# Performance work log

Measured on AMD Instinct MI355X. Metric: run time of the kernel, lower is better.

Reference implementation:

```python
import jax, jax.numpy as jnp
import numpy as np

B, LP, LR = 16, 128, 1024
D = 128
DG = 640  # 5 * 128 concat
K = 7     # number of FC trans heads
EDGE_P = 0.05


def _gcn_block(x, adj, mask, W1, b1, W2, b2):
    # x: [B,L,DG], adj: [B,L,L] (nonzero => edge weight 1, like dense_to_sparse + GCNConv)
    A = (adj != 0).astype(x.dtype)
    L = A.shape[-1]
    eye = jnp.eye(L, dtype=x.dtype)
    Ah = jnp.maximum(A, eye)                     # add_remaining_self_loops
    deg = Ah.sum(axis=1)                         # col degree [B,L] (gcn_norm uses target index)
    dinv = jax.lax.rsqrt(deg)                    # deg >= 1 thanks to self loops
    N = Ah * dinv[:, :, None] * dinv[:, None, :] # normalized adjacency per edge (r,c)
    agg = lambda h: jnp.einsum('brc,brd->bcd', N, h)  # aggregate sources r into target c
    h1 = jax.nn.relu(agg(x @ W1) + b1)
    h2 = agg(h1 @ W2) + b2
    return jax.nn.relu(x + h2) * mask[..., None]


def _fc_trans(feature, Wt, bt):
    # feature: [B,L,DG]; Wt: [K,D,DG]; bt: [K,D]
    h = jnp.einsum('bld,kod->kblo', feature, Wt) + bt[:, None, None, :]
    h = jax.nn.relu(h)                 # FCNet [640->128], ReLU (dropout off in eval)
    return jnp.swapaxes(h, 2, 3)       # [K,B,D,L] (transpose(1,2))


def _forward(x_pep, x_ss_pep, x_2_pep, x_dense_pep, x_pretrain_pep,
             x_pro, x_ss_pro, x_2_pro, x_dense_pro, x_pretrain_pro,
             x_edge_pep, x_edge_pro, x_seqmask_pep, x_seqmask_pro,
             E_seq, E_ss, E_two, W_dpep, b_dpep, W_dpro, b_dpro,
             W_ppep, b_ppep, W_ppro, b_ppro,
             Wg_pep1, bg_pep1, Wg_pep2, bg_pep2,
             Wg_pro1, bg_pro1, Wg_pro2, bg_pro2,
             Wt_pep, bt_pep, Wt_pro, bt_pro):
    enc_pep = jnp.concatenate([
        E_seq[x_pep], E_ss[x_ss_pep], E_two[x_2_pep],
        x_dense_pep @ W_dpep + b_dpep,
        x_pretrain_pep @ W_ppep + b_ppep], axis=-1) * x_seqmask_pep[..., None]
    enc_pro = jnp.concatenate([
        E_seq[x_pro], E_ss[x_ss_pro], E_two[x_2_pro],
        x_dense_pro @ W_dpro + b_dpro,
        x_pretrain_pro @ W_ppro + b_ppro], axis=-1) * x_seqmask_pro[..., None]

    f_pep = _gcn_block(enc_pep, x_edge_pep, x_seqmask_pep, Wg_pep1, bg_pep1, Wg_pep2, bg_pep2)
    f_pro = _gcn_block(enc_pro, x_edge_pro, x_seqmask_pro, Wg_pro1, bg_pro1, Wg_pro2, bg_pro2)

    pep_vecs = _fc_trans(f_pep, Wt_pep, bt_pep)[..., None]        # [K,B,D,LP,1] (unsqueeze 3)
    pro_vecs = _fc_trans(f_pro, Wt_pro, bt_pro)[:, :, :, None, :]  # [K,B,D,1,LR] (unsqueeze 2)
    return pep_vecs, pro_vecs


def setup_inputs() -> dict:
    key = jax.random.key(0)
    ks = jax.random.split(key, 40)
    f32 = jnp.float32
    s = 0.05
    inp = {
        'x_pep': jax.random.randint(ks[0], (B, LP), 0, 25),
        'x_ss_pep': jax.random.randint(ks[1], (B, LP), 0, 73),
        'x_2_pep': jax.random.randint(ks[2], (B, LP), 0, 8),
        'x_dense_pep': jax.random.normal(ks[3], (B, LP, 3), f32),
        'x_pretrain_pep': jax.random.normal(ks[4], (B, LP, 1024), f32),
        'x_pro': jax.random.randint(ks[5], (B, LR), 0, 25),
        'x_ss_pro': jax.random.randint(ks[6], (B, LR), 0, 73),
        'x_2_pro': jax.random.randint(ks[7], (B, LR), 0, 8),
        'x_dense_pro': jax.random.normal(ks[8], (B, LR, 23), f32),
        'x_pretrain_pro': jax.random.normal(ks[9], (B, LR, 1024), f32),
        'x_edge_pep': (jax.random.uniform(ks[10], (B, LP, LP)) < EDGE_P).astype(f32),
        'x_edge_pro': (jax.random.uniform(ks[11], (B, LR, LR)) < EDGE_P).astype(f32),
        'x_seqmask_pep': jnp.ones((B, LP), f32),
        'x_seqmask_pro': jnp.ones((B, LR), f32),
        'E_seq': jax.random.normal(ks[12], (25, D), f32) * s,
        'E_ss': jax.random.normal(ks[13], (73, D), f32) * s,
        'E_two': jax.random.normal(ks[14], (8, D), f32) * s,
        'W_dpep': jax.random.normal(ks[15], (3, D), f32) * s,
        'b_dpep': jnp.zeros((D,), f32),
        'W_dpro': jax.random.normal(ks[16], (23, D), f32) * s,
        'b_dpro': jnp.zeros((D,), f32),
        'W_ppep': jax.random.normal(ks[17], (1024, D), f32) * s,
        'b_ppep': jnp.zeros((D,), f32),
        'W_ppro': jax.random.normal(ks[18], (1024, D), f32) * s,
        'b_ppro': jnp.zeros((D,), f32),
        'Wg_pep1': jax.random.normal(ks[19], (DG, DG), f32) * s,
        'bg_pep1': jnp.zeros((DG,), f32),
        'Wg_pep2': jax.random.normal(ks[20], (DG, DG), f32) * s,
        'bg_pep2': jnp.zeros((DG,), f32),
        'Wg_pro1': jax.random.normal(ks[21], (DG, DG), f32) * s,
        'bg_pro1': jnp.zeros((DG,), f32),
        'Wg_pro2': jax.random.normal(ks[22], (DG, DG), f32) * s,
        'bg_pro2': jnp.zeros((DG,), f32),
        'Wt_pep': jax.random.normal(ks[23], (K, D, DG), f32) * s,
        'bt_pep': jnp.zeros((K, D), f32),
        'Wt_pro': jax.random.normal(ks[24], (K, D, DG), f32) * s,
        'bt_pro': jnp.zeros((K, D), f32),
    }
    return inp


def reference(x_pep, x_ss_pep, x_2_pep, x_dense_pep, x_pretrain_pep,
              x_pro, x_ss_pro, x_2_pro, x_dense_pro, x_pretrain_pro,
              x_edge_pep, x_edge_pro, x_seqmask_pep, x_seqmask_pro,
              E_seq, E_ss, E_two, W_dpep, b_dpep, W_dpro, b_dpro,
              W_ppep, b_ppep, W_ppro, b_ppro,
              Wg_pep1, bg_pep1, Wg_pep2, bg_pep2,
              Wg_pro1, bg_pro1, Wg_pro2, bg_pro2,
              Wt_pep, bt_pep, Wt_pro, bt_pro):
    return _forward(x_pep, x_ss_pep, x_2_pep, x_dense_pep, x_pretrain_pep,
                    x_pro, x_ss_pro, x_2_pro, x_dense_pro, x_pretrain_pro,
                    x_edge_pep, x_edge_pro, x_seqmask_pep, x_seqmask_pro,
                    E_seq, E_ss, E_two, W_dpep, b_dpep, W_dpro, b_dpro,
                    W_ppep, b_ppep, W_ppro, b_ppro,
                    Wg_pep1, bg_pep1, Wg_pep2, bg_pep2,
                    Wg_pro1, bg_pro1, Wg_pro2, bg_pro2,
                    Wt_pep, bt_pep, Wt_pro, bt_pro)
```

## Files before the change

kernel.cpp:

```cpp
#include <hip/hip_runtime.h>
#include <hip/hip_bf16.h>

#define BSZ 16
#define LP 128
#define LR 1024
#define DD 128
#define DG 640
#define KH 7
#define SPLITK 4

typedef __bf16 bf16x8 __attribute__((ext_vector_type(8)));
typedef __bf16 bf16x4v __attribute__((ext_vector_type(4)));
typedef float f32x4 __attribute__((ext_vector_type(4)));
typedef unsigned int uint32;

__device__ __forceinline__ void gl16(const void* g, void* l) {
  __builtin_amdgcn_global_load_lds(
      (const __attribute__((address_space(1))) unsigned int*)g,
      (__attribute__((address_space(3))) unsigned int*)l, 16, 0, 0);
}

__device__ __forceinline__ void mfma_core_lds(
    const ushort* __restrict__ Ab, int lda,
    const ushort* __restrict__ Bb, int ldb,
    int m0, int n0, int kStart, int kEnd, f32x4 (&acc)[4][4]) {
  __shared__ __align__(16) ushort As[128 * 64];
  __shared__ __align__(16) ushort Bs[128 * 64];
  int t = threadIdx.x;
  int wave = t >> 6, lane = t & 63;
  int quad = lane >> 4, l16 = lane & 15;
  int wm = (wave >> 1) * 64, wn = (wave & 1) * 64;

  int row0 = (wave * 256 + lane) >> 3;
  int s0 = lane & 7;
  const ushort* aBase = Ab + (size_t)(m0 + row0) * lda + s0 * 8;
  const ushort* bBase = Bb + (size_t)(n0 + row0) * ldb + s0 * 8;

  for (int k0 = kStart; k0 < kEnd; k0 += 64) {
    #pragma unroll
    for (int i = 0; i < 4; ++i) {
      gl16(aBase + (size_t)i * 8 * lda + k0, &As[wave * 2048 + i * 512]);
      gl16(bBase + (size_t)i * 8 * ldb + k0, &Bs[wave * 2048 + i * 512]);
    }
    __syncthreads();
    #pragma unroll
    for (int kc = 0; kc < 2; ++kc) {
      bf16x8 af[4], bfr[4];
      #pragma unroll
      for (int fi = 0; fi < 4; ++fi)
        af[fi] = *(const bf16x8*)&As[(wm + fi * 16 + l16) * 64 + kc * 32 + quad * 8];
      #pragma unroll
      for (int fj = 0; fj < 4; ++fj)
        bfr[fj] = *(const bf16x8*)&Bs[(wn + fj * 16 + l16) * 64 + kc * 32 + quad * 8];
      #pragma unroll
      for (int fi = 0; fi < 4; ++fi)
        #pragma unroll
        for (int fj = 0; fj < 4; ++fj)
          acc[fi][fj] = __builtin_amdgcn_mfma_f32_16x16x32_bf16(
              af[fi], bfr[fj], acc[fi][fj], 0, 0, 0);
    }
    __syncthreads();
  }
}

__device__ __forceinline__ void mfma_core_f32(
    const float* __restrict__ Af, int lda,
    const ushort* __restrict__ Bb, int ldb,
    int m0, int n0, int kStart, int kEnd, f32x4 (&acc)[4][4]) {
  __shared__ __align__(16) ushort As[128 * 72];
  __shared__ __align__(16) ushort Bs[128 * 72];
  int t = threadIdx.x;
  int wave = t >> 6, lane = t & 63;
  int quad = lane >> 4, l16 = lane & 15;
  int wm = (wave >> 1) * 64, wn = (wave & 1) * 64;
  int r1 = t >> 2, o1 = (t & 3) * 16;

  int4 b00, b01, b10, b11;
  float4 af32[8];

  auto load_k = [&](int k0) {
    b00 = *(const int4*)(Bb + (size_t)(n0 + r1) * ldb + k0 + o1);
    b01 = *(const int4*)(Bb + (size_t)(n0 + r1) * ldb + k0 + o1 + 8);
    b10 = *(const int4*)(Bb + (size_t)(n0 + r1 + 64) * ldb + k0 + o1);
    b11 = *(const int4*)(Bb + (size_t)(n0 + r1 + 64) * ldb + k0 + o1 + 8);
    #pragma unroll
    for (int s = 0; s < 8; ++s) {
      int idx = t + s * 256;
      int row = idx >> 4, c4 = (idx & 15) * 4;
      af32[s] = *(const float4*)(Af + (size_t)(m0 + row) * lda + k0 + c4);
    }
  };

  load_k(kStart);
  for (int k0 = kStart; k0 < kEnd; k0 += 64) {
    __syncthreads();
    #pragma unroll
    for (int s = 0; s < 8; ++s) {
      int idx = t + s * 256;
      int row = idx >> 4, c4 = (idx & 15) * 4;
      ushort4 u; __bf16 h;
      h = (__bf16)af32[s].x; u.x = *(ushort*)&h;
      h = (__bf16)af32[s].y; u.y = *(ushort*)&h;
      h = (__bf16)af32[s].z; u.z = *(ushort*)&h;
      h = (__bf16)af32[s].w; u.w = *(ushort*)&h;
      *(ushort4*)&As[row * 72 + c4] = u;
    }
    *(int4*)&Bs[r1 * 72 + o1] = b00;
    *(int4*)&Bs[r1 * 72 + o1 + 8] = b01;
    *(int4*)&Bs[(r1 + 64) * 72 + o1] = b10;
    *(int4*)&Bs[(r1 + 64) * 72 + o1 + 8] = b11;
    __syncthreads();
    if (k0 + 64 < kEnd) load_k(k0 + 64);
    #pragma unroll
    for (int kc = 0; kc < 2; ++kc) {
      bf16x8 af[4], bfr[4];
      #pragma unroll
      for (int fi = 0; fi < 4; ++fi)
        af[fi] = *(const bf16x8*)&As[(wm + fi * 16 + l16) * 72 + kc * 32 + quad * 8];
      #pragma unroll
      for (int fj = 0; fj < 4; ++fj)
        bfr[fj] = *(const bf16x8*)&Bs[(wn + fj * 16 + l16) * 72 + kc * 32 + quad * 8];
      #pragma unroll
      for (int fi = 0; fi < 4; ++fi)
        #pragma unroll
        for (int fj = 0; fj < 4; ++fj)
          acc[fi][fj] = __builtin_amdgcn_mfma_f32_16x16x32_bf16(
              af[fi], bfr[fj], acc[fi][fj], 0, 0, 0);
    }
  }
}

__device__ __forceinline__ void agg_core(
    const uint32* __restrict__ pb, int L,
    const ushort* __restrict__ Bb, int ldb,
    int m0, int n0, f32x4 (&acc)[4][4]) {
  __shared__ __align__(16) ushort Bs[128 * 64];
  __shared__ uint32 Aw[2][128];
  int t = threadIdx.x;
  int wave = t >> 6, lane = t & 63;
  int quad = lane >> 4, l16 = lane & 15;
  int wm = (wave >> 1) * 64, wn = (wave & 1) * 64;
  int half = t >> 7, cc = t & 127;

  int row0 = (wave * 256 + lane) >> 3;
  int s0 = lane & 7;
  const ushort* bBase = Bb + (size_t)(n0 + row0) * ldb + s0 * 8;
  const uint32* pbBase = pb + (size_t)half * L + m0 + cc;

  for (int k0 = 0; k0 < L; k0 += 64) {
    #pragma unroll
    for (int i = 0; i < 4; ++i)
      gl16(bBase + (size_t)i * 8 * ldb + k0, &Bs[wave * 2048 + i * 512]);
    Aw[half][cc] = pbBase[(size_t)(k0 >> 5) * L];
    __syncthreads();
    #pragma unroll
    for (int kc = 0; kc < 2; ++kc) {
      bf16x8 af[4], bfr[4];
      #pragma unroll
      for (int fj = 0; fj < 4; ++fj)
        bfr[fj] = *(const bf16x8*)&Bs[(wn + fj * 16 + l16) * 64 + kc * 32 + quad * 8];
      #pragma unroll
      for (int fi = 0; fi < 4; ++fi) {
        uint32 bits = (Aw[kc][wm + fi * 16 + l16] >> (quad * 8)) & 0xffu;
        int4 p;
        p.x = (int)((((bits >> 0) & 1) ? 0x3F80u : 0u) | (((bits >> 1) & 1) ? 0x3F800000u : 0u));
        p.y = (int)((((bits >> 2) & 1) ? 0x3F80u : 0u) | (((bits >> 3) & 1) ? 0x3F800000u : 0u));
        p.z = (int)((((bits >> 4) & 1) ? 0x3F80u : 0u) | (((bits >> 5) & 1) ? 0x3F800000u : 0u));
        p.w = (int)((((bits >> 6) & 1) ? 0x3F80u : 0u) | (((bits >> 7) & 1) ? 0x3F800000u : 0u));
        af[fi] = *(bf16x8*)&p;
      }
      #pragma unroll
      for (int fi = 0; fi < 4; ++fi)
        #pragma unroll
        for (int fj = 0; fj < 4; ++fj)
          acc[fi][fj] = __builtin_amdgcn_mfma_f32_16x16x32_bf16(
              af[fi], bfr[fj], acc[fi][fj], 0, 0, 0);
    }
    __syncthreads();
  }
}

__device__ __forceinline__ void tr_tile(const float* __restrict__ src,
                                        __bf16* __restrict__ dst,
                                        int R, int C, int cb, int rb, int t) {
  __shared__ float T[32][33];
  int r0 = rb * 32, c0 = cb * 32;
  #pragma unroll
  for (int s = 0; s < 4; ++s) {
    int idx = t + s * 256;
    int r = idx >> 5, c = idx & 31;
    T[r][c] = src[(size_t)(r0 + r) * C + c0 + c];
  }
  __syncthreads();
  #pragma unroll
  for (int s = 0; s < 4; ++s) {
    int idx = t + s * 256;
    int c = idx >> 5, r = idx & 31;
    dst[(size_t)(c0 + c) * R + r0 + r] = (__bf16)T[r][c];
  }
}

__global__ __launch_bounds__(256) void prep_weights(
    const float* __restrict__ Wppep, const float* __restrict__ Wppro,
    const float* __restrict__ Wg1p, const float* __restrict__ Wg2p,
    const float* __restrict__ Wg1r, const float* __restrict__ Wg2r,
    const float* __restrict__ Wtp, const float* __restrict__ Wtr,
    __bf16* __restrict__ WppTp, __bf16* __restrict__ WppTr,
    __bf16* __restrict__ Wg1Tp, __bf16* __restrict__ Wg2Tp,
    __bf16* __restrict__ Wg1Tr, __bf16* __restrict__ Wg2Tr,
    __bf16* __restrict__ WtBp, __bf16* __restrict__ WtBr) {
  int z = blockIdx.z, bx = blockIdx.x, t = threadIdx.x;
  if (z < 2) {
    if (bx >= 128) return;
    tr_tile(z ? Wppro : Wppep, z ? WppTr : WppTp, 1024, 128, bx % 4, bx / 4, t);
  } else if (z < 6) {
    if (bx >= 400) return;
    const float* src = (z == 2) ? Wg1p : (z == 3) ? Wg2p : (z == 4) ? Wg1r : Wg2r;
    __bf16* dst = (z == 2) ? Wg1Tp : (z == 3) ? Wg2Tp : (z == 4) ? Wg1Tr : Wg2Tr;
    tr_tile(src, dst, 640, 640, bx % 20, bx / 20, t);
  } else {
    if (bx >= 560) return;
    const float* src = (z == 6) ? Wtp : Wtr;
    __bf16* dst = (z == 6) ? WtBp : WtBr;
    int i = bx * 256 + t;
    float4 v = ((const float4*)src)[i];
    bf16x4v o;
    o.x = (__bf16)v.x; o.y = (__bf16)v.y; o.z = (__bf16)v.z; o.w = (__bf16)v.w;
    ((bf16x4v*)dst)[i] = o;
  }
}

__global__ __launch_bounds__(256) void zero_f32(float* __restrict__ p, int n) {
  int i = blockIdx.x * 256 + threadIdx.x;
  if (i < n) p[i] = 0.f;
}

__global__ __launch_bounds__(256) void rsqrt_k(const float* __restrict__ deg,
                                               float* __restrict__ dinv, int n) {
  int i = blockIdx.x * 256 + threadIdx.x;
  if (i < n) dinv[i] = rsqrtf(deg[i]);
}

__global__ __launch_bounds__(256) void prep_pack_merged(
    const float* __restrict__ adjP, const float* __restrict__ adjR,
    uint32* __restrict__ packedP, uint32* __restrict__ packedR,
    float* __restrict__ degP, float* __restrict__ degR) {
  int t = threadIdx.x;
  const float* adj; uint32* packed; float* deg;
  int b, rw, c, L;
  if (blockIdx.z < 16) {
    L = LR; b = blockIdx.z; rw = blockIdx.y; c = blockIdx.x * 256 + t;
    adj = adjR; packed = packedR; deg = degR;
  } else {
    L = LP; b = blockIdx.y; rw = blockIdx.x; c = t;
    if (b >= 16 || c >= LP) return;
    adj = adjP; packed = packedP; deg = degP;
  }
  const float* adjB = adj + (size_t)b * L * L;
  uint32 w = 0;
  int rbase = rw * 32;
  #pragma unroll 8
  for (int j = 0; j < 32; ++j) {
    float a = adjB[(size_t)(rbase + j) * L + c];
    if (a != 0.f || (rbase + j) == c) w |= (1u << j);
  }
  packed[((size_t)b * (L >> 5) + rw) * L + c] = w;
  atomicAdd(deg + b * L + c, (float)__popc(w));
}

__global__ __launch_bounds__(256) void pre_gemm(
    const float* __restrict__ XpP, const float* __restrict__ XpR,
    const __bf16* __restrict__ WppTp, const __bf16* __restrict__ WppTr,
    float* __restrict__ partP, float* __restrict__ partR) {
  int bx = blockIdx.x, s = blockIdx.y;
  int pep = bx < (BSZ * LP / 128);
  int m0 = (pep ? bx : bx - BSZ * LP / 128) * 128;
  const float* A = pep ? XpP : XpR;
  const ushort* B = (const ushort*)(pep ? WppTp : WppTr);
  int BL = pep ? BSZ * LP : BSZ * LR;
  float* part = (pep ? partP : partR) + (size_t)s * BL * DD;

  f32x4 acc[4][4];
  #pragma unroll
  for (int i = 0; i < 4; ++i)
    #pragma unroll
    for (int j = 0; j < 4; ++j) acc[i][j] = (f32x4){0.f, 0.f, 0.f, 0.f};
  mfma_core_f32(A, 1024, B, 1024, m0, 0, s * (1024 / SPLITK),
                (s + 1) * (1024 / SPLITK), acc);

  int t = threadIdx.x;
  int wave = t >> 6, lane = t & 63;
  int quad = lane >> 4, l16 = lane & 15;
  int wm = (wave >> 1) * 64, wn = (wave & 1) * 64;
  #pragma unroll
  for (int fi = 0; fi < 4; ++fi)
    #pragma unroll
    for (int r = 0; r < 4; ++r) {
      int m = m0 + wm + fi * 16 + quad * 4 + r;
      #pragma unroll
      for (int fj = 0; fj < 4; ++fj) {
        int n = wn + fj * 16 + l16;
        part[(size_t)m * DD + n] = acc[fi][fj][r];
      }
    }
}

__global__ __launch_bounds__(128) void encoder_merged(
    const int* __restrict__ xsP, const int* __restrict__ xssP,
    const int* __restrict__ x2P, const float* __restrict__ xdP,
    const float* __restrict__ WdP, const float* __restrict__ bdP,
    const float* __restrict__ maskP, const float* __restrict__ partP,
    const float* __restrict__ bppP, __bf16* __restrict__ encP,
    const int* __restrict__ xsR, const int* __restrict__ xssR,
    const int* __restrict__ x2R, const float* __restrict__ xdR,
    const float* __restrict__ WdR, const float* __restrict__ bdR,
    const float* __restrict__ maskR, const float* __restrict__ partR,
    const float* __restrict__ bppR, __bf16* __restrict__ encR,
    const float* __restrict__ Eseq, const float* __restrict__ Ess,
    const float* __restrict__ Etwo) {
  int gw = blockIdx.x;
  int t = threadIdx.x;
  int pep = gw < BSZ * LP;
  int row = pep ? gw : gw - BSZ * LP;
  int BL = pep ? BSZ * LP : BSZ * LR;
  int Kd = pep ? 3 : 23;
  const int* xs = pep ? xsP : xsR;
  const int* xss = pep ? xssP : xssR;
  const int* x2 = pep ? x2P : x2R;
  const float* xd = pep ? xdP : xdR;
  const float* Wd = pep ? WdP : WdR;
  const float* bd = pep ? bdP : bdR;
  const float* mask = pep ? maskP : maskR;
  const float* part = pep ? partP : partR;
  const float* bpp = pep ? bppP : bppR;
  __bf16* enc = pep ? encP : encR;

  float m = mask[row];
  int i0 = xs[row], i1 = xss[row], i2 = x2[row];
  __bf16* e = enc + (size_t)row * DG;
  e[t]        = (__bf16)(Eseq[i0 * DD + t] * m);
  e[DD + t]   = (__bf16)(Ess[i1 * DD + t] * m);
  e[2*DD + t] = (__bf16)(Etwo[i2 * DD + t] * m);
  float acc = bd[t];
  const float* xr = xd + (size_t)row * Kd;
  for (int i = 0; i < Kd; ++i) acc = fmaf(xr[i], Wd[i * DD + t], acc);
  e[3*DD + t] = (__bf16)(acc * m);
  float p = bpp[t];
  #pragma unroll
  for (int s = 0; s < SPLITK; ++s)
    p += part[(size_t)s * BL * DD + (size_t)row * DD + t];
  e[4*DD + t] = (__bf16)(p * m);
}

__global__ __launch_bounds__(256) void linT_merged(
    const __bf16* __restrict__ WgTp, const __bf16* __restrict__ srcP,
    const float* __restrict__ dinvP, __bf16* __restrict__ dstP,
    const __bf16* __restrict__ WgTr, const __bf16* __restrict__ srcR,
    const float* __restrict__ dinvR, __bf16* __restrict__ dstR) {
  int bx = blockIdx.x;
  int pep = bx < (BSZ * LP / 128);
  int n0 = (pep ? bx : bx - BSZ * LP / 128) * 128;
  int m0 = blockIdx.y * 128;
  int BL = pep ? BSZ * LP : BSZ * LR;
  const ushort* A = (const ushort*)(pep ? WgTp : WgTr);
  const ushort* B = (const ushort*)(pep ? srcP : srcR);
  const float* dinv = pep ? dinvP : dinvR;
  __bf16* dst = pep ? dstP : dstR;

  f32x4 acc[4][4];
  #pragma unroll
  for (int i = 0; i < 4; ++i)
    #pragma unroll
    for (int j = 0; j < 4; ++j) acc[i][j] = (f32x4){0.f, 0.f, 0.f, 0.f};
  mfma_core_lds(A, DG, B, DG, m0, n0, 0, DG, acc);

  int t = threadIdx.x;
  int wave = t >> 6, lane = t & 63;
  int quad = lane >> 4, l16 = lane & 15;
  int wm = (wave >> 1) * 64, wn = (wave & 1) * 64;
  #pragma unroll
  for (int fi = 0; fi < 4; ++fi)
    #pragma unroll
    for (int r = 0; r < 4; ++r) {
      int m = m0 + wm + fi * 16 + quad * 4 + r;
      #pragma unroll
      for (int fj = 0; fj < 4; ++fj) {
        int n = n0 + wn + fj * 16 + l16;
        dst[(size_t)m * BL + n] = (__bf16)(acc[fi][fj][r] * dinv[n]);
      }
    }
}

__global__ __launch_bounds__(256) void agg_merged(
    const uint32* __restrict__ packedP, const __bf16* __restrict__ XtP,
    const float* __restrict__ dinvP, const float* __restrict__ biasP,
    const __bf16* __restrict__ encEP, const float* __restrict__ maskP,
    __bf16* __restrict__ YP,
    const uint32* __restrict__ packedR, const __bf16* __restrict__ XtR,
    const float* __restrict__ dinvR, const float* __restrict__ biasR,
    const __bf16* __restrict__ encER, const float* __restrict__ maskR,
    __bf16* __restrict__ YR) {
  int bx = blockIdx.x;
  int b = bx / 5;
  int n0 = (bx % 5) * 128;
  int pep = (blockIdx.y == 0);
  int L = pep ? LP : LR;
  int BL = BSZ * L;
  int m0 = pep ? 0 : (blockIdx.y - 1) * 128;
  const uint32* pb = (pep ? packedP : packedR) + (size_t)b * (L >> 5) * L;
  const ushort* Bb = (const ushort*)(pep ? XtP : XtR) + (size_t)b * L;
  const float* dinv = pep ? dinvP : dinvR;
  const float* bias = pep ? biasP : biasR;
  const __bf16* encE = pep ? encEP : encER;
  const float* mask = pep ? maskP : maskR;
  __bf16* Y = pep ? YP : YR;

  f32x4 acc[4][4];
  #pragma unroll
  for (int i = 0; i < 4; ++i)
    #pragma unroll
    for (int j = 0; j < 4; ++j) acc[i][j] = (f32x4){0.f, 0.f, 0.f, 0.f};
  agg_core(pb, L, Bb, BL, m0, n0, acc);

  int t = threadIdx.x;
  int wave = t >> 6, lane = t & 63;
  int quad = lane >> 4, l16 = lane & 15;
  int wm = (wave >> 1) * 64, wn = (wave & 1) * 64;
  int gRow = b * L;
  #pragma unroll
  for (int fi = 0; fi < 4; ++fi)
    #pragma unroll
    for (int r = 0; r < 4; ++r) {
      int m = m0 + wm + fi * 16 + quad * 4 + r;
      int gi = gRow + m;
      float di = dinv[gi];
      float rm = mask ? mask[gi] : 1.f;
      #pragma unroll
      for (int fj = 0; fj < 4; ++fj) {
        int n = n0 + wn + fj * 16 + l16;
        float v = acc[fi][fj][r] * di + bias[n];
        if (encE) v += (float)encE[(size_t)gi * DG + n];
        v = fmaxf(v, 0.f);
        v *= rm;
        Y[(size_t)gi * DG + n] = (__bf16)v;
      }
    }
}

__global__ __launch_bounds__(256) void fct_merged(
    const __bf16* __restrict__ WtBp, const float* __restrict__ btp,
    const __bf16* __restrict__ Yp, float* __restrict__ outP,
    const __bf16* __restrict__ WtBr, const float* __restrict__ btr,
    const __bf16* __restrict__ Yr, float* __restrict__ outR) {
  int kh = blockIdx.y;
  int pro = (blockIdx.z < 16);
  const ushort* A;
  const ushort* B;
  const float* bt;
  int n0;
  if (pro) {
    A = (const ushort*)(WtBr + (size_t)kh * DD * DG);
    B = (const ushort*)(Yr + (size_t)blockIdx.z * LR * DG);
    bt = btr;
    n0 = blockIdx.x * 128;
  } else {
    A = (const ushort*)(WtBp + (size_t)kh * DD * DG);
    B = (const ushort*)Yp;
    bt = btp;
    n0 = ((blockIdx.z - 16) * 8 + blockIdx.x) * 128;
  }

  f32x4 acc[4][4];
  #pragma unroll
  for (int i = 0; i < 4; ++i)
    #pragma unroll
    for (int j = 0; j < 4; ++j) acc[i][j] = (f32x4){0.f, 0.f, 0.f, 0.f};
  mfma_core_lds(A, DG, B, DG, 0, n0, 0, DG, acc);

  int t = threadIdx.x;
  int wave = t >> 6, lane = t & 63;
  int quad = lane >> 4, l16 = lane & 15;
  int wm = (wave >> 1) * 64, wn = (wave & 1) * 64;
  #pragma unroll
  for (int fi = 0; fi < 4; ++fi)
    #pragma unroll
    for (int r = 0; r < 4; ++r) {
      int m = wm + fi * 16 + quad * 4 + r;
      float bb = bt[kh * DD + m];
      #pragma unroll
      for (int fj = 0; fj < 4; ++fj) {
        int n = n0 + wn + fj * 16 + l16;
        float v = fmaxf(acc[fi][fj][r] + bb, 0.f);
        if (pro) {
          outR[((size_t)(kh * BSZ + blockIdx.z) * DD + m) * LR + n] = v;
        } else {
          int b = n >> 7, l = n & 127;
          outP[((size_t)(kh * BSZ + b) * DD + m) * LP + l] = v;
        }
      }
    }
}

extern "C" void kernel_launch(void* const* d_in, const int* in_sizes, int n_in,
                              void* d_out, int out_size, void* d_ws, size_t ws_size,
                              hipStream_t stream) {
  const int*   x_pep          = (const int*)d_in[0];
  const int*   x_ss_pep       = (const int*)d_in[1];
  const int*   x_2_pep        = (const int*)d_in[2];
  const float* x_dense_pep    = (const float*)d_in[3];
  const float* x_pretrain_pep = (const float*)d_in[4];
  const int*   x_pro          = (const int*)d_in[5];
  const int*   x_ss_pro       = (const int*)d_in[6];
  const int*   x_2_pro        = (const int*)d_in[7];
  const float* x_dense_pro    = (const float*)d_in[8];
  const float* x_pretrain_pro = (const float*)d_in[9];
  const float* x_edge_pep     = (const float*)d_in[10];
  const float* x_edge_pro     = (const float*)d_in[11];
  const float* mask_pep       = (const float*)d_in[12];
  const float* mask_pro       = (const float*)d_in[13];
  const float* E_seq          = (const float*)d_in[14];
  const float* E_ss           = (const float*)d_in[15];
  const float* E_two          = (const float*)d_in[16];
  const float* W_dpep         = (const float*)d_in[17];
  const float* b_dpep         = (const float*)d_in[18];
  const float* W_dpro         = (const float*)d_in[19];
  const float* b_dpro         = (const float*)d_in[20];
  const float* W_ppep         = (const float*)d_in[21];
  const float* b_ppep         = (const float*)d_in[22];
  const float* W_ppro         = (const float*)d_in[23];
  const float* b_ppro         = (const float*)d_in[24];
  const float* Wg_pep1        = (const float*)d_in[25];
  const float* bg_pep1        = (const float*)d_in[26];
  const float* Wg_pep2        = (const float*)d_in[27];
  const float* bg_pep2        = (const float*)d_in[28];
  const float* Wg_pro1        = (const float*)d_in[29];
  const float* bg_pro1        = (const float*)d_in[30];
  const float* Wg_pro2        = (const float*)d_in[31];
  const float* bg_pro2        = (const float*)d_in[32];
  const float* Wt_pep         = (const float*)d_in[33];
  const float* bt_pep         = (const float*)d_in[34];
  const float* Wt_pro         = (const float*)d_in[35];
  const float* bt_pro         = (const float*)d_in[36];

  float* out = (float*)d_out;
  const int BLp = BSZ * LP;
  const int BLr = BSZ * LR;
  const size_t out_pro_off = (size_t)KH * BSZ * DD * LP;

  char* w = (char*)d_ws;
  __bf16* encBp  = (__bf16*)w; w += (size_t)BLp * DG * 2;
  __bf16* encBr  = (__bf16*)w; w += (size_t)BLr * DG * 2;
  __bf16* bufATp = (__bf16*)w; w += (size_t)DG * BLp * 2;
  __bf16* bufATr = (__bf16*)w; w += (size_t)DG * BLr * 2;
  __bf16* bufYp  = (__bf16*)w; w += (size_t)BLp * DG * 2;
  __bf16* bufYr  = (__bf16*)w; w += (size_t)BLr * DG * 2;
  __bf16* WppTp  = (__bf16*)w; w += (size_t)DD * 1024 * 2;
  __bf16* WppTr  = (__bf16*)w; w += (size_t)DD * 1024 * 2;
  __bf16* Wg1Tp  = (__bf16*)w; w += (size_t)DG * DG * 2;
  __bf16* Wg2Tp  = (__bf16*)w; w += (size_t)DG * DG * 2;
  __bf16* Wg1Tr  = (__bf16*)w; w += (size_t)DG * DG * 2;
  __bf16* Wg2Tr  = (__bf16*)w; w += (size_t)DG * DG * 2;
  __bf16* WtBp   = (__bf16*)w; w += (size_t)KH * DD * DG * 2;
  __bf16* WtBr   = (__bf16*)w; w += (size_t)KH * DD * DG * 2;
  uint32* packedP = (uint32*)w; w += (size_t)BSZ * (LP / 32) * LP * 4;
  uint32* packedR = (uint32*)w; w += (size_t)BSZ * (LR / 32) * LR * 4;
  float* degP  = (float*)w; w += (size_t)BLp * 4;
  float* degR  = (float*)w; w += (size_t)BLr * 4;
  float* dinvP = (float*)w; w += (size_t)BLp * 4;
  float* dinvR = (float*)w; w += (size_t)BLr * 4;
  float* partP = (float*)w; w += (size_t)SPLITK * BLp * DD * 4;
  float* partR = (float*)w; w += (size_t)SPLITK * BLr * DD * 4;

  prep_weights<<<dim3(560, 1, 8), 256, 0, stream>>>(
      W_ppep, W_ppro, Wg_pep1, Wg_pep2, Wg_pro1, Wg_pro2, Wt_pep, Wt_pro,
      WppTp, WppTr, Wg1Tp, Wg2Tp, Wg1Tr, Wg2Tr, WtBp, WtBr);
  zero_f32<<<(BLp + BLr) / 256, 256, 0, stream>>>(degP, BLp + BLr);
  prep_pack_merged<<<dim3(4, 32, 17), 256, 0, stream>>>(
      x_edge_pep, x_edge_pro, packedP, packedR, degP, degR);
  rsqrt_k<<<(BLp + BLr) / 256, 256, 0, stream>>>(degP, dinvP, BLp + BLr);
  pre_gemm<<<dim3((BLp + BLr) / 128, SPLITK), 256, 0, stream>>>(
      x_pretrain_pep, x_pretrain_pro, WppTp, WppTr, partP, partR);
  encoder_merged<<<BLp + BLr, 128, 0, stream>>>(
      x_pep, x_ss_pep, x_2_pep, x_dense_pep, W_dpep, b_dpep, mask_pep, partP,
      b_ppep, encBp,
      x_pro, x_ss_pro, x_2_pro, x_dense_pro, W_dpro, b_dpro, mask_pro, partR,
      b_ppro, encBr,
      E_seq, E_ss, E_two);
  linT_merged<<<dim3((BLp + BLr) / 128, DG / 128), 256, 0, stream>>>(
      Wg1Tp, encBp, dinvP, bufATp, Wg1Tr, encBr, dinvR, bufATr);
  agg_merged<<<dim3(80, 9), 256, 0, stream>>>(
      packedP, bufATp, dinvP, bg_pep1, nullptr, nullptr, bufYp,
      packedR, bufATr, dinvR, bg_pro1, nullptr, nullptr, bufYr);
  linT_merged<<<dim3((BLp + BLr) / 128, DG / 128), 256, 0, stream>>>(
      Wg2Tp, bufYp, dinvP, bufATp, Wg2Tr, bufYr, dinvR, bufATr);
  agg_merged<<<dim3(80, 9), 256, 0, stream>>>(
      packedP, bufATp, dinvP, bg_pep2, encBp, mask_pep, bufYp,
      packedR, bufATr, dinvR, bg_pro2, encBr, mask_pro, bufYr);
  fct_merged<<<dim3(LR / 128, KH, 18), 256, 0, stream>>>(
      WtBp, bt_pep, bufYp, out,
      WtBr, bt_pro, bufYr, out + out_pro_off);
}
```

Measured before the change: 495.8 us.

## Halve GEMM N-tile to 64 and switch to register-prefetched padded LDS staging

Replaces the 128x128 MFMA tiles in the linear, aggregation and FC-trans kernels with 128x64 tiles, doubling grid sizes so more blocks fill the GPU. It also drops the direct global-to-LDS loads in favour of register prefetch of the next K slice, stored into padded (stride 72) LDS to avoid bank conflicts and overlap loads with MFMA compute. The cost is lower per-block data reuse, so each operand is read from memory more often.

```diff
diff --git a/kernel.cpp b/kernel.cpp
--- a/kernel.cpp
+++ b/kernel.cpp
@@ -14,52 +14,110 @@
 typedef float f32x4 __attribute__((ext_vector_type(4)));
 typedef unsigned int uint32;
 
-__device__ __forceinline__ void gl16(const void* g, void* l) {
-  __builtin_amdgcn_global_load_lds(
-      (const __attribute__((address_space(1))) unsigned int*)g,
-      (__attribute__((address_space(3))) unsigned int*)l, 16, 0, 0);
-}
-
-__device__ __forceinline__ void mfma_core_lds(
+__device__ __forceinline__ void mfma_core_n64(
     const ushort* __restrict__ Ab, int lda,
     const ushort* __restrict__ Bb, int ldb,
-    int m0, int n0, int kStart, int kEnd, f32x4 (&acc)[4][4]) {
-  __shared__ __align__(16) ushort As[128 * 64];
-  __shared__ __align__(16) ushort Bs[128 * 64];
+    int m0, int n0, int kStart, int kEnd, f32x4 (&acc)[2][4]) {
+  __shared__ __align__(16) ushort As[128 * 72];
+  __shared__ __align__(16) ushort Bs[64 * 72];
   int t = threadIdx.x;
   int wave = t >> 6, lane = t & 63;
   int quad = lane >> 4, l16 = lane & 15;
-  int wm = (wave >> 1) * 64, wn = (wave & 1) * 64;
-
-  int row0 = (wave * 256 + lane) >> 3;
-  int s0 = lane & 7;
-  const ushort* aBase = Ab + (size_t)(m0 + row0) * lda + s0 * 8;
-  const ushort* bBase = Bb + (size_t)(n0 + row0) * ldb + s0 * 8;
-
+  int wm = wave * 32;
+  int r1 = t >> 2, o1 = (t & 3) * 16;
+
+  int4 a0, a1, a2, a3, bb0, bb1;
+  auto load_k = [&](int k0) {
+    a0 = *(const int4*)(Ab + (size_t)(m0 + r1) * lda + k0 + o1);
+    a1 = *(const int4*)(Ab + (size_t)(m0 + r1) * lda + k0 + o1 + 8);
+    a2 = *(const int4*)(Ab + (size_t)(m0 + r1 + 64) * lda + k0 + o1);
+    a3 = *(const int4*)(Ab + (size_t)(m0 + r1 + 64) * lda + k0 + o1 + 8);
+    bb0 = *(const int4*)(Bb + (size_t)(n0 + r1) * ldb + k0 + o1);
+    bb1 = *(const int4*)(Bb + (size_t)(n0 + r1) * ldb + k0 + o1 + 8);
+  };
+
+  load_k(kStart);
   for (int k0 = kStart; k0 < kEnd; k0 += 64) {
-    #pragma unroll
-    for (int i = 0; i < 4; ++i) {
-      gl16(aBase + (size_t)i * 8 * lda + k0, &As[wave * 2048 + i * 512]);
-      gl16(bBase + (size_t)i * 8 * ldb + k0, &Bs[wave * 2048 + i * 512]);
-    }
     __syncthreads();
+    *(int4*)&As[r1 * 72 + o1] = a0;
+    *(int4*)&As[r1 * 72 + o1 + 8] = a1;
+    *(int4*)&As[(r1 + 64) * 72 + o1] = a2;
+    *(int4*)&As[(r1 + 64) * 72 + o1 + 8] = a3;
+    *(int4*)&Bs[r1 * 72 + o1] = bb0;
+    *(int4*)&Bs[r1 * 72 + o1 + 8] = bb1;
+    __syncthreads();
+    if (k0 + 64 < kEnd) load_k(k0 + 64);
     #pragma unroll
     for (int kc = 0; kc < 2; ++kc) {
-      bf16x8 af[4], bfr[4];
-      #pragma unroll
-      for (int fi = 0; fi < 4; ++fi)
-        af[fi] = *(const bf16x8*)&As[(wm + fi * 16 + l16) * 64 + kc * 32 + quad * 8];
+      bf16x8 af[2], bfr[4];
+      #pragma unroll
+      for (int fi = 0; fi < 2; ++fi)
+        af[fi] = *(const bf16x8*)&As[(wm + fi * 16 + l16) * 72 + kc * 32 + quad * 8];
       #pragma unroll
       for (int fj = 0; fj < 4; ++fj)
-        bfr[fj] = *(const bf16x8*)&Bs[(wn + fj * 16 + l16) * 64 + kc * 32 + quad * 8];
-      #pragma unroll
-      for (int fi = 0; fi < 4; ++fi)
+        bfr[fj] = *(const bf16x8*)&Bs[(fj * 16 + l16) * 72 + kc * 32 + quad * 8];
+      #pragma unroll
+      for (int fi = 0; fi < 2; ++fi)
         #pragma unroll
         for (int fj = 0; fj < 4; ++fj)
           acc[fi][fj] = __builtin_amdgcn_mfma_f32_16x16x32_bf16(
               af[fi], bfr[fj], acc[fi][fj], 0, 0, 0);
     }
+  }
+}
+
+__device__ __forceinline__ void agg_core_n64(
+    const uint32* __restrict__ pb, int L,
+    const ushort* __restrict__ Bb, int ldb,
+    int m0, int n0, f32x4 (&acc)[2][4]) {
+  __shared__ __align__(16) ushort Bs[64 * 72];
+  __shared__ uint32 Aw[2][128];
+  int t = threadIdx.x;
+  int wave = t >> 6, lane = t & 63;
+  int quad = lane >> 4, l16 = lane & 15;
+  int wm = wave * 32;
+  int r1 = t >> 2, o1 = (t & 3) * 16;
+  int half = t >> 7, cc = t & 127;
+
+  int4 bb0, bb1;
+  uint32 w;
+  auto load_k = [&](int k0) {
+    bb0 = *(const int4*)(Bb + (size_t)(n0 + r1) * ldb + k0 + o1);
+    bb1 = *(const int4*)(Bb + (size_t)(n0 + r1) * ldb + k0 + o1 + 8);
+    w = pb[(size_t)((k0 >> 5) + half) * L + m0 + cc];
+  };
+
+  load_k(0);
+  for (int k0 = 0; k0 < L; k0 += 64) {
     __syncthreads();
+    *(int4*)&Bs[r1 * 72 + o1] = bb0;
+    *(int4*)&Bs[r1 * 72 + o1 + 8] = bb1;
+    Aw[half][cc] = w;
+    __syncthreads();
+    if (k0 + 64 < L) load_k(k0 + 64);
+    #pragma unroll
+    for (int kc = 0; kc < 2; ++kc) {
+      bf16x8 af[2], bfr[4];
+      #pragma unroll
+      for (int fj = 0; fj < 4; ++fj)
+        bfr[fj] = *(const bf16x8*)&Bs[(fj * 16 + l16) * 72 + kc * 32 + quad * 8];
+      #pragma unroll
+      for (int fi = 0; fi < 2; ++fi) {
+        uint32 bits = (Aw[kc][wm + fi * 16 + l16] >> (quad * 8)) & 0xffu;
+        int4 p;
+        p.x = (int)((((bits >> 0) & 1) ? 0x3F80u : 0u) | (((bits >> 1) & 1) ? 0x3F800000u : 0u));
+        p.y = (int)((((bits >> 2) & 1) ? 0x3F80u : 0u) | (((bits >> 3) & 1) ? 0x3F800000u : 0u));
+        p.z = (int)((((bits >> 4) & 1) ? 0x3F80u : 0u) | (((bits >> 5) & 1) ? 0x3F800000u : 0u));
+        p.w = (int)((((bits >> 6) & 1) ? 0x3F80u : 0u) | (((bits >> 7) & 1) ? 0x3F800000u : 0u));
+        af[fi] = *(bf16x8*)&p;
+      }
+      #pragma unroll
+      for (int fi = 0; fi < 2; ++fi)
+        #pragma unroll
+        for (int fj = 0; fj < 4; ++fj)
+          acc[fi][fj] = __builtin_amdgcn_mfma_f32_16x16x32_bf16(
+              af[fi], bfr[fj], acc[fi][fj], 0, 0, 0);
+    }
   }
 }
 
@@ -127,56 +185,6 @@
           acc[fi][fj] = __builtin_amdgcn_mfma_f32_16x16x32_bf16(
               af[fi], bfr[fj], acc[fi][fj], 0, 0, 0);
     }
-  }
-}
-
-__device__ __forceinline__ void agg_core(
-    const uint32* __restrict__ pb, int L,
-    const ushort* __restrict__ Bb, int ldb,
-    int m0, int n0, f32x4 (&acc)[4][4]) {
-  __shared__ __align__(16) ushort Bs[128 * 64];
-  __shared__ uint32 Aw[2][128];
-  int t = threadIdx.x;
-  int wave = t >> 6, lane = t & 63;
-  int quad = lane >> 4, l16 = lane & 15;
-  int wm = (wave >> 1) * 64, wn = (wave & 1) * 64;
-  int half = t >> 7, cc = t & 127;
-
-  int row0 = (wave * 256 + lane) >> 3;
-  int s0 = lane & 7;
-  const ushort* bBase = Bb + (size_t)(n0 + row0) * ldb + s0 * 8;
-  const uint32* pbBase = pb + (size_t)half * L + m0 + cc;
-
-  for (int k0 = 0; k0 < L; k0 += 64) {
-    #pragma unroll
-    for (int i = 0; i < 4; ++i)
-      gl16(bBase + (size_t)i * 8 * ldb + k0, &Bs[wave * 2048 + i * 512]);
-    Aw[half][cc] = pbBase[(size_t)(k0 >> 5) * L];
-    __syncthreads();
-    #pragma unroll
-    for (int kc = 0; kc < 2; ++kc) {
-      bf16x8 af[4], bfr[4];
-      #pragma unroll
-      for (int fj = 0; fj < 4; ++fj)
-        bfr[fj] = *(const bf16x8*)&Bs[(wn + fj * 16 + l16) * 64 + kc * 32 + quad * 8];
-      #pragma unroll
-      for (int fi = 0; fi < 4; ++fi) {
-        uint32 bits = (Aw[kc][wm + fi * 16 + l16] >> (quad * 8)) & 0xffu;
-        int4 p;
-        p.x = (int)((((bits >> 0) & 1) ? 0x3F80u : 0u) | (((bits >> 1) & 1) ? 0x3F800000u : 0u));
-        p.y = (int)((((bits >> 2) & 1) ? 0x3F80u : 0u) | (((bits >> 3) & 1) ? 0x3F800000u : 0u));
-        p.z = (int)((((bits >> 4) & 1) ? 0x3F80u : 0u) | (((bits >> 5) & 1) ? 0x3F800000u : 0u));
-        p.w = (int)((((bits >> 6) & 1) ? 0x3F80u : 0u) | (((bits >> 7) & 1) ? 0x3F800000u : 0u));
-        af[fi] = *(bf16x8*)&p;
-      }
-      #pragma unroll
-      for (int fi = 0; fi < 4; ++fi)
-        #pragma unroll
-        for (int fj = 0; fj < 4; ++fj)
-          acc[fi][fj] = __builtin_amdgcn_mfma_f32_16x16x32_bf16(
-              af[fi], bfr[fj], acc[fi][fj], 0, 0, 0);
-    }
-    __syncthreads();
   }
 }
 
@@ -358,8 +366,8 @@
     const __bf16* __restrict__ WgTr, const __bf16* __restrict__ srcR,
     const float* __restrict__ dinvR, __bf16* __restrict__ dstR) {
   int bx = blockIdx.x;
-  int pep = bx < (BSZ * LP / 128);
-  int n0 = (pep ? bx : bx - BSZ * LP / 128) * 128;
+  int pep = bx < (BSZ * LP / 64);
+  int n0 = (pep ? bx : bx - BSZ * LP / 64) * 64;
   int m0 = blockIdx.y * 128;
   int BL = pep ? BSZ * LP : BSZ * LR;
   const ushort* A = (const ushort*)(pep ? WgTp : WgTr);
@@ -367,25 +375,25 @@
   const float* dinv = pep ? dinvP : dinvR;
   __bf16* dst = pep ? dstP : dstR;
 
-  f32x4 acc[4][4];
-  #pragma unroll
-  for (int i = 0; i < 4; ++i)
+  f32x4 acc[2][4];
+  #pragma unroll
+  for (int i = 0; i < 2; ++i)
     #pragma unroll
     for (int j = 0; j < 4; ++j) acc[i][j] = (f32x4){0.f, 0.f, 0.f, 0.f};
-  mfma_core_lds(A, DG, B, DG, m0, n0, 0, DG, acc);
+  mfma_core_n64(A, DG, B, DG, m0, n0, 0, DG, acc);
 
   int t = threadIdx.x;
   int wave = t >> 6, lane = t & 63;
   int quad = lane >> 4, l16 = lane & 15;
-  int wm = (wave >> 1) * 64, wn = (wave & 1) * 64;
-  #pragma unroll
-  for (int fi = 0; fi < 4; ++fi)
+  int wm = wave * 32;
+  #pragma unroll
+  for (int fi = 0; fi < 2; ++fi)
     #pragma unroll
     for (int r = 0; r < 4; ++r) {
       int m = m0 + wm + fi * 16 + quad * 4 + r;
       #pragma unroll
       for (int fj = 0; fj < 4; ++fj) {
-        int n = n0 + wn + fj * 16 + l16;
+        int n = n0 + fj * 16 + l16;
         dst[(size_t)m * BL + n] = (__bf16)(acc[fi][fj][r] * dinv[n]);
       }
     }
@@ -401,8 +409,8 @@
     const __bf16* __restrict__ encER, const float* __restrict__ maskR,
     __bf16* __restrict__ YR) {
   int bx = blockIdx.x;
-  int b = bx / 5;
-  int n0 = (bx % 5) * 128;
+  int b = bx / 10;
+  int n0 = (bx % 10) * 64;
   int pep = (blockIdx.y == 0);
   int L = pep ? LP : LR;
   int BL = BSZ * L;
@@ -415,20 +423,20 @@
   const float* mask = pep ? maskP : maskR;
   __bf16* Y = pep ? YP : YR;
 
-  f32x4 acc[4][4];
-  #pragma unroll
-  for (int i = 0; i < 4; ++i)
+  f32x4 acc[2][4];
+  #pragma unroll
+  for (int i = 0; i < 2; ++i)
     #pragma unroll
     for (int j = 0; j < 4; ++j) acc[i][j] = (f32x4){0.f, 0.f, 0.f, 0.f};
-  agg_core(pb, L, Bb, BL, m0, n0, acc);
+  agg_core_n64(pb, L, Bb, BL, m0, n0, acc);
 
   int t = threadIdx.x;
   int wave = t >> 6, lane = t & 63;
   int quad = lane >> 4, l16 = lane & 15;
-  int wm = (wave >> 1) * 64, wn = (wave & 1) * 64;
+  int wm = wave * 32;
   int gRow = b * L;
   #pragma unroll
-  for (int fi = 0; fi < 4; ++fi)
+  for (int fi = 0; fi < 2; ++fi)
     #pragma unroll
     for (int r = 0; r < 4; ++r) {
       int m = m0 + wm + fi * 16 + quad * 4 + r;
@@ -437,7 +445,7 @@
       float rm = mask ? mask[gi] : 1.f;
       #pragma unroll
       for (int fj = 0; fj < 4; ++fj) {
-        int n = n0 + wn + fj * 16 + l16;
+        int n = n0 + fj * 16 + l16;
         float v = acc[fi][fj][r] * di + bias[n];
         if (encE) v += (float)encE[(size_t)gi * DG + n];
         v = fmaxf(v, 0.f);
@@ -462,34 +470,34 @@
     A = (const ushort*)(WtBr + (size_t)kh * DD * DG);
     B = (const ushort*)(Yr + (size_t)blockIdx.z * LR * DG);
     bt = btr;
-    n0 = blockIdx.x * 128;
+    n0 = blockIdx.x * 64;
   } else {
     A = (const ushort*)(WtBp + (size_t)kh * DD * DG);
     B = (const ushort*)Yp;
     bt = btp;
-    n0 = ((blockIdx.z - 16) * 8 + blockIdx.x) * 128;
-  }
-
-  f32x4 acc[4][4];
-  #pragma unroll
-  for (int i = 0; i < 4; ++i)
+    n0 = ((blockIdx.z - 16) * 16 + blockIdx.x) * 64;
+  }
+
+  f32x4 acc[2][4];
+  #pragma unroll
+  for (int i = 0; i < 2; ++i)
     #pragma unroll
     for (int j = 0; j < 4; ++j) acc[i][j] = (f32x4){0.f, 0.f, 0.f, 0.f};
-  mfma_core_lds(A, DG, B, DG, 0, n0, 0, DG, acc);
+  mfma_core_n64(A, DG, B, DG, 0, n0, 0, DG, acc);
 
   int t = threadIdx.x;
   int wave = t >> 6, lane = t & 63;
   int quad = lane >> 4, l16 = lane & 15;
-  int wm = (wave >> 1) * 64, wn = (wave & 1) * 64;
-  #pragma unroll
-  for (int fi = 0; fi < 4; ++fi)
+  int wm = wave * 32;
+  #pragma unroll
+  for (int fi = 0; fi < 2; ++fi)
     #pragma unroll
     for (int r = 0; r < 4; ++r) {
       int m = wm + fi * 16 + quad * 4 + r;
       float bb = bt[kh * DD + m];
       #pragma unroll
       for (int fj = 0; fj < 4; ++fj) {
-        int n = n0 + wn + fj * 16 + l16;
+        int n = n0 + fj * 16 + l16;
         float v = fmaxf(acc[fi][fj][r] + bb, 0.f);
         if (pro) {
           outR[((size_t)(kh * BSZ + blockIdx.z) * DD + m) * LR + n] = v;
@@ -586,17 +594,17 @@
       x_pro, x_ss_pro, x_2_pro, x_dense_pro, W_dpro, b_dpro, mask_pro, partR,
       b_ppro, encBr,
       E_seq, E_ss, E_two);
-  linT_merged<<<dim3((BLp + BLr) / 128, DG / 128), 256, 0, stream>>>(
+  linT_merged<<<dim3((BLp + BLr) / 64, DG / 128), 256, 0, stream>>>(
       Wg1Tp, encBp, dinvP, bufATp, Wg1Tr, encBr, dinvR, bufATr);
-  agg_merged<<<dim3(80, 9), 256, 0, stream>>>(
+  agg_merged<<<dim3(160, 9), 256, 0, stream>>>(
       packedP, bufATp, dinvP, bg_pep1, nullptr, nullptr, bufYp,
       packedR, bufATr, dinvR, bg_pro1, nullptr, nullptr, bufYr);
-  linT_merged<<<dim3((BLp + BLr) / 128, DG / 128), 256, 0, stream>>>(
+  linT_merged<<<dim3((BLp + BLr) / 64, DG / 128), 256, 0, stream>>>(
       Wg2Tp, bufYp, dinvP, bufATp, Wg2Tr, bufYr, dinvR, bufATr);
-  agg_merged<<<dim3(80, 9), 256, 0, stream>>>(
+  agg_merged<<<dim3(160, 9), 256, 0, stream>>>(
       packedP, bufATp, dinvP, bg_pep2, encBp, mask_pep, bufYp,
       packedR, bufATr, dinvR, bg_pro2, encBr, mask_pro, bufYr);
-  fct_merged<<<dim3(LR / 128, KH, 18), 256, 0, stream>>>(
+  fct_merged<<<dim3(16, KH, 18), 256, 0, stream>>>(
       WtBp, bt_pep, bufYp, out,
       WtBr, bt_pro, bufYr, out + out_pro_off);
 }
```

New measurement: 452.2 us. 8.8% less time.
